# Kernel tuning notes

Hardware: AMD Instinct MI355X
Metric: run time of the kernel (lower is better)

## Reference

```python
import jax, jax.numpy as jnp
import numpy as np

D_MODEL = 4096
NUM_HEADS = 32
D_K = D_MODEL // NUM_HEADS  # 128
SEQ = D_K  # module's final `O @ scores` requires h*seq == O.shape[1] == d_model -> seq == d_k
WSCALE = 0.02


def setup_inputs() -> dict:
    key = jax.random.key(0)
    kq, kk, kv, ko, kx = jax.random.split(key, 5)
    Q = jax.random.normal(kq, (D_MODEL, D_MODEL), jnp.float32) * WSCALE
    K = jax.random.normal(kk, (D_MODEL, D_MODEL), jnp.float32) * WSCALE
    V = jax.random.normal(kv, (D_MODEL, D_MODEL), jnp.float32) * WSCALE
    O = jax.random.normal(ko, (D_MODEL, D_MODEL), jnp.float32) * WSCALE
    x = jax.random.normal(kx, (SEQ, D_MODEL), jnp.float32)
    return {"Q": Q, "K": K, "V": V, "O": O, "x": x}


def reference(Q, K, V, O, x):
    h, d = NUM_HEADS, D_K
    seq = x.shape[0]
    # stack and split weights into per-head projections: (3, h, d, d_in)
    qkv_w = jnp.stack((Q, K, V), axis=0).reshape(3, h, d, -1)
    # project: (3, h, seq, d)
    proj = jnp.einsum('phdi,si->phsd', qkv_w, x)
    q_proj, k_proj, v_proj = proj[0], proj[1], proj[2]
    # attention scores: (h, seq, seq)
    scores = jnp.einsum('hqd,hkd->hqk', q_proj, k_proj) / jnp.sqrt(jnp.asarray(d, scores_dtype := q_proj.dtype))
    # module uses triu (upper-triangular incl. diagonal) mask, multiply then fill zeros with -inf
    mask = jnp.triu(jnp.ones((seq, seq), dtype=scores.dtype))
    masked = mask * scores
    masked = jnp.where(masked == 0.0, -jnp.inf, masked)
    # stable softmax over keys (single exp, same math as subtract-max softmax)
    shifted = masked - jnp.max(masked, axis=-1, keepdims=True)
    e = jnp.exp(shifted)
    probs = e / jnp.sum(e, axis=-1, keepdims=True)
    # attention output: (h, seq, d)
    att = jnp.einsum('hqk,hkd->hqd', probs, v_proj)
    # module flattens (h, seq) together: ((h*seq), d), then left-multiplies by O
    att = att.reshape(h * seq, d)
    return O @ att  # (d_model, d_k)
```

## Files before the change

### kernel.cpp

```cpp
#include <hip/hip_runtime.h>
#include <stdint.h>

#define DM 4096

typedef __attribute__((ext_vector_type(4))) float f32x4;
typedef __attribute__((ext_vector_type(8))) short s16x8;
typedef __attribute__((ext_vector_type(8))) unsigned short u16x8;
typedef __attribute__((ext_vector_type(4))) unsigned short u16x4;

__device__ __forceinline__ unsigned short f2bf(float f) {
  union { float f; unsigned u; } c; c.f = f;
  unsigned u = c.u;
  u += 0x7FFFu + ((u >> 16) & 1u);
  return (unsigned short)(u >> 16);
}
__device__ __forceinline__ float bf2f(unsigned short h) {
  union { unsigned u; float f; } c; c.u = ((unsigned)h) << 16;
  return c.f;
}

__device__ __forceinline__ void splitbf(float v, short& hi, short& lo) {
  union { float f; unsigned u; } c; c.f = v;
  unsigned uh = c.u & 0xFFFF0000u;
  hi = (short)(uh >> 16);
  union { unsigned u; float f; } d; d.u = uh;
  lo = (short)f2bf(v - d.f);
}

__device__ __forceinline__ void wave_barrier_lgkm() {
  asm volatile("s_waitcnt lgkmcnt(0)" ::: "memory");
  __builtin_amdgcn_s_barrier();
}

__global__ __launch_bounds__(256) void k0_xsplit(const float* __restrict__ x,
                                                 unsigned short* __restrict__ xh) {
  int g = blockIdx.x * 256 + threadIdx.x;
  int kg = g & 511, s = g >> 9;
  const float* px = x + (size_t)s * DM + kg * 8;
  f32x4 v0 = *(const f32x4*)px;
  f32x4 v1 = *(const f32x4*)(px + 4);
  u16x8 hi;
#pragma unroll
  for (int j = 0; j < 8; ++j) {
    float v = (j < 4) ? v0[j] : v1[j - 4];
    hi[j] = f2bf(v);
  }
  *(u16x8*)(xh + ((size_t)kg * 128 + s) * 8) = hi;
}

__global__ __launch_bounds__(256) void k1_proj(const float* __restrict__ Q,
                                               const float* __restrict__ K,
                                               const float* __restrict__ V,
                                               const unsigned short* __restrict__ xh,
                                               float* __restrict__ pp) {
  __shared__ __align__(16) unsigned short xs[4096];
  int bid = blockIdx.x;
  int rb = bid >> 1, kc = bid & 1;
  int r0 = rb * 64;
  int w = r0 >> 12;
  int rloc = r0 & 4095;
  const float* W = (w == 0) ? Q : ((w == 1) ? K : V);
  int tid = threadIdx.x;
  int wave = tid >> 6, lane = tid & 63;
  int l15 = lane & 15, lg = lane >> 4;
  int rwb = rloc + wave * 16;
  const float* arow = W + (size_t)(rwb + l15) * DM + lg * 8;
  int kbase = kc * 2048;
  f32x4 acc[8];
#pragma unroll
  for (int i = 0; i < 8; ++i) acc[i] = (f32x4)0.f;

  u16x8 xb[4][2];
  f32x4 ab[4][2];
#pragma unroll
  for (int p = 0; p < 4; ++p) {
    int kk = kbase + p * 32;
    const u16x8* s = (const u16x8*)(xh + (size_t)kk * 128);
    xb[p][0] = s[tid];
    xb[p][1] = s[256 + tid];
    ab[p][0] = *(const f32x4*)(arow + kk);
    ab[p][1] = *(const f32x4*)(arow + kk + 4);
  }

  for (int tt = 0; tt < 16; ++tt) {
#pragma unroll
    for (int p = 0; p < 4; ++p) {
      int t = tt * 4 + p;
      wave_barrier_lgkm();
      ((u16x8*)xs)[tid] = xb[p][0];
      ((u16x8*)xs)[256 + tid] = xb[p][1];
      s16x8 Ahi, Alo;
#pragma unroll
      for (int j = 0; j < 8; ++j) {
        float v = (j < 4) ? ab[p][0][j] : ab[p][1][j - 4];
        short h, l; splitbf(v, h, l);
        Ahi[j] = h; Alo[j] = l;
      }
      int tp = t + 4;
      int kkp = kbase + ((tp < 64) ? tp : 0) * 32;
      {
        const u16x8* s = (const u16x8*)(xh + (size_t)kkp * 128);
        xb[p][0] = s[tid];
        xb[p][1] = s[256 + tid];
        ab[p][0] = *(const f32x4*)(arow + kkp);
        ab[p][1] = *(const f32x4*)(arow + kkp + 4);
      }
      wave_barrier_lgkm();
#pragma unroll
      for (int nt = 0; nt < 8; ++nt) {
        s16x8 bh = *(const s16x8*)&xs[((lg * 128) + nt * 16 + l15) * 8];
        acc[nt] = __builtin_amdgcn_mfma_f32_16x16x32_bf16(Ahi, bh, acc[nt], 0, 0, 0);
        acc[nt] = __builtin_amdgcn_mfma_f32_16x16x32_bf16(Alo, bh, acc[nt], 0, 0, 0);
      }
    }
  }

  int h = rwb >> 7;
  int dbase = (rwb & 127) + (lg << 2);
  size_t base = (size_t)(kc * 3 + w) * 524288;
  if (w < 2) {
#pragma unroll
    for (int nt = 0; nt < 8; ++nt) {
      int s = nt * 16 + l15;
      *(f32x4*)(pp + base + (size_t)(h * 128 + s) * 128 + dbase) = acc[nt];
    }
  } else {
#pragma unroll
    for (int nt = 0; nt < 8; ++nt) {
      int s = nt * 16 + l15;
#pragma unroll
      for (int r = 0; r < 4; ++r)
        pp[base + (size_t)(h * 128 + dbase + r) * 128 + s] = acc[nt][r];
    }
  }
}

__global__ __launch_bounds__(256) void k2_attn(const float* __restrict__ pp,
                                               unsigned short* __restrict__ att) {
  __shared__ __align__(16) unsigned short lds[32768];
  int h = blockIdx.x;
  int tid = threadIdx.x, wave = tid >> 6, lane = tid & 63;
  int l15 = lane & 15, lg = lane >> 4;
  const float* pk0 = pp + (size_t)1 * 524288 + (size_t)h * 16384;
  const float* pk1 = pp + (size_t)4 * 524288 + (size_t)h * 16384;
  const float* pv0 = pp + (size_t)2 * 524288 + (size_t)h * 16384;
  const float* pv1 = pp + (size_t)5 * 524288 + (size_t)h * 16384;
  for (int g = tid; g < 2048; g += 256) {
    int dg = g & 15, k = g >> 4;
    size_t so = (size_t)k * 128 + dg * 8;
    f32x4 u0 = *(const f32x4*)(pk0 + so);
    f32x4 u1 = *(const f32x4*)(pk0 + so + 4);
    f32x4 w0 = *(const f32x4*)(pk1 + so);
    f32x4 w1 = *(const f32x4*)(pk1 + so + 4);
    u16x8 kb;
#pragma unroll
    for (int j = 0; j < 4; ++j) {
      kb[j] = f2bf(u0[j] + w0[j]);
      kb[4 + j] = f2bf(u1[j] + w1[j]);
    }
    *(u16x8*)&lds[(size_t)(dg * 128 + k) * 8] = kb;
    int kg = g & 15, d = g >> 4;
    size_t vo = (size_t)d * 128 + kg * 8;
    f32x4 x0 = *(const f32x4*)(pv0 + vo);
    f32x4 x1 = *(const f32x4*)(pv0 + vo + 4);
    f32x4 y0 = *(const f32x4*)(pv1 + vo);
    f32x4 y1 = *(const f32x4*)(pv1 + vo + 4);
    u16x8 vb;
#pragma unroll
    for (int j = 0; j < 4; ++j) {
      vb[j] = f2bf(x0[j] + y0[j]);
      vb[4 + j] = f2bf(x1[j] + y1[j]);
    }
    *(u16x8*)&lds[16384 + (size_t)(kg * 128 + d) * 8] = vb;
  }
  __syncthreads();

  int qbase = wave * 32;
  const float* pq0 = pp + (size_t)h * 16384;
  const float* pq1 = pp + (size_t)3 * 524288 + (size_t)h * 16384;
  const float RS = 0.08838834764831845f;
  f32x4 sc[2][8];
#pragma unroll
  for (int a = 0; a < 2; ++a)
#pragma unroll
    for (int b = 0; b < 8; ++b) sc[a][b] = (f32x4)0.f;

  for (int ks = 0; ks < 4; ++ks) {
    s16x8 qhi[2], qlo[2];
#pragma unroll
    for (int qt = 0; qt < 2; ++qt) {
      int q = qbase + qt * 16 + l15;
      size_t qo = (size_t)q * 128 + ks * 32 + lg * 8;
      f32x4 u0 = *(const f32x4*)(pq0 + qo);
      f32x4 u1 = *(const f32x4*)(pq0 + qo + 4);
      f32x4 w0 = *(const f32x4*)(pq1 + qo);
      f32x4 w1 = *(const f32x4*)(pq1 + qo + 4);
#pragma unroll
      for (int j = 0; j < 8; ++j) {
        float v = ((j < 4) ? (u0[j] + w0[j]) : (u1[j - 4] + w1[j - 4])) * RS;
        unsigned short hh = f2bf(v);
        qhi[qt][j] = (short)hh;
        qlo[qt][j] = (short)f2bf(v - bf2f(hh));
      }
    }
#pragma unroll
    for (int nt = 0; nt < 8; ++nt) {
      s16x8 kb = *(const s16x8*)&lds[(size_t)((ks * 4 + lg) * 128 + nt * 16 + l15) * 8];
#pragma unroll
      for (int qt = 0; qt < 2; ++qt) {
        sc[qt][nt] = __builtin_amdgcn_mfma_f32_16x16x32_bf16(qhi[qt], kb, sc[qt][nt], 0, 0, 0);
        sc[qt][nt] = __builtin_amdgcn_mfma_f32_16x16x32_bf16(qlo[qt], kb, sc[qt][nt], 0, 0, 0);
      }
    }
  }
  float inv[2][4];
#pragma unroll
  for (int qt = 0; qt < 2; ++qt) {
#pragma unroll
    for (int r = 0; r < 4; ++r) {
      int q = qbase + qt * 16 + (lg << 2) + r;
      float m = -3.0e38f;
#pragma unroll
      for (int nt = 0; nt < 8; ++nt) {
        int k = nt * 16 + l15;
        float v = sc[qt][nt][r];
        if (k >= q) m = fmaxf(m, v);
      }
#pragma unroll
      for (int d = 1; d < 16; d <<= 1) m = fmaxf(m, __shfl_xor(m, d));
      float ssum = 0.f;
#pragma unroll
      for (int nt = 0; nt < 8; ++nt) {
        int k = nt * 16 + l15;
        float v = sc[qt][nt][r];
        float e = (k >= q) ? __expf(v - m) : 0.f;
        sc[qt][nt][r] = e;
        ssum += e;
      }
#pragma unroll
      for (int d = 1; d < 16; d <<= 1) ssum += __shfl_xor(ssum, d);
      inv[qt][r] = 1.f / ssum;
    }
  }
  __syncthreads();
#pragma unroll
  for (int qt = 0; qt < 2; ++qt)
#pragma unroll
    for (int nt = 0; nt < 8; ++nt) {
      int k = nt * 16 + l15;
#pragma unroll
      for (int r = 0; r < 4; ++r) {
        int q = qbase + qt * 16 + (lg << 2) + r;
        lds[(size_t)((k >> 3) * 128 + q) * 8 + (k & 7)] = f2bf(sc[qt][nt][r] * inv[qt][r]);
      }
    }
  __syncthreads();
  f32x4 o[2][8];
#pragma unroll
  for (int a = 0; a < 2; ++a)
#pragma unroll
    for (int b = 0; b < 8; ++b) o[a][b] = (f32x4)0.f;
  for (int ks = 0; ks < 4; ++ks) {
    s16x8 pa[2];
#pragma unroll
    for (int qt = 0; qt < 2; ++qt)
      pa[qt] = *(const s16x8*)&lds[(size_t)((ks * 4 + lg) * 128 + qbase + qt * 16 + l15) * 8];
#pragma unroll
    for (int nt = 0; nt < 8; ++nt) {
      s16x8 vb = *(const s16x8*)&lds[16384 + (size_t)((ks * 4 + lg) * 128 + nt * 16 + l15) * 8];
      o[0][nt] = __builtin_amdgcn_mfma_f32_16x16x32_bf16(pa[0], vb, o[0][nt], 0, 0, 0);
      o[1][nt] = __builtin_amdgcn_mfma_f32_16x16x32_bf16(pa[1], vb, o[1][nt], 0, 0, 0);
    }
  }
#pragma unroll
  for (int qt = 0; qt < 2; ++qt)
#pragma unroll
    for (int nt = 0; nt < 8; ++nt) {
      int c = nt * 16 + l15;
      int jq = h * 128 + qbase + qt * 16 + (lg << 2);
      u16x4 pk;
#pragma unroll
      for (int r = 0; r < 4; ++r) pk[r] = f2bf(o[qt][nt][r]);
      *(u16x4*)(att + (size_t)(jq >> 3) * 1024 + c * 8 + (jq & 7)) = pk;
    }
}

__global__ __launch_bounds__(256) void k3_out(const float* __restrict__ O,
                                              const unsigned short* __restrict__ att,
                                              float* __restrict__ out) {
  __shared__ __align__(16) unsigned short ats[4096];
  int bid = blockIdx.x;
  int rb = bid >> 3, kc = bid & 7;
  int r0 = rb * 64;
  int kbase = kc * 512;
  int tid = threadIdx.x, wave = tid >> 6, lane = tid & 63;
  int l15 = lane & 15, lg = lane >> 4;
  int rwb = r0 + wave * 16;
  const float* arow = O + (size_t)(rwb + l15) * DM + lg * 8;
  f32x4 acc[8];
#pragma unroll
  for (int i = 0; i < 8; ++i) acc[i] = (f32x4)0.f;

  u16x8 bb[4][2];
  f32x4 ab[4][2];
#pragma unroll
  for (int p = 0; p < 4; ++p) {
    int kk = kbase + p * 32;
    const u16x8* s = (const u16x8*)(att + (size_t)(kk >> 3) * 1024);
    bb[p][0] = s[tid];
    bb[p][1] = s[256 + tid];
    ab[p][0] = *(const f32x4*)(arow + kk);
    ab[p][1] = *(const f32x4*)(arow + kk + 4);
  }

  for (int tt = 0; tt < 4; ++tt) {
#pragma unroll
    for (int p = 0; p < 4; ++p) {
      int t = tt * 4 + p;
      wave_barrier_lgkm();
      ((u16x8*)ats)[tid] = bb[p][0];
      ((u16x8*)ats)[256 + tid] = bb[p][1];
      s16x8 Ahi, Alo;
#pragma unroll
      for (int j = 0; j < 8; ++j) {
        float v = (j < 4) ? ab[p][0][j] : ab[p][1][j - 4];
        short h, l; splitbf(v, h, l);
        Ahi[j] = h; Alo[j] = l;
      }
      int tp = t + 4;
      int kkp = kbase + ((tp < 16) ? tp : 0) * 32;
      {
        const u16x8* s = (const u16x8*)(att + (size_t)(kkp >> 3) * 1024);
        bb[p][0] = s[tid];
        bb[p][1] = s[256 + tid];
        ab[p][0] = *(const f32x4*)(arow + kkp);
        ab[p][1] = *(const f32x4*)(arow + kkp + 4);
      }
      wave_barrier_lgkm();
#pragma unroll
      for (int nt = 0; nt < 8; ++nt) {
        s16x8 bh = *(const s16x8*)&ats[((lg * 128) + nt * 16 + l15) * 8];
        acc[nt] = __builtin_amdgcn_mfma_f32_16x16x32_bf16(Ahi, bh, acc[nt], 0, 0, 0);
        acc[nt] = __builtin_amdgcn_mfma_f32_16x16x32_bf16(Alo, bh, acc[nt], 0, 0, 0);
      }
    }
  }
#pragma unroll
  for (int nt = 0; nt < 8; ++nt) {
#pragma unroll
    for (int r = 0; r < 4; ++r) {
      int row = rwb + (lg << 2) + r;
      atomicAdd(&out[(size_t)row * 128 + nt * 16 + l15], acc[nt][r]);
    }
  }
}

extern "C" void kernel_launch(void* const* d_in, const int* in_sizes, int n_in,
                              void* d_out, int out_size, void* d_ws, size_t ws_size,
                              hipStream_t stream) {
  const float* Q = (const float*)d_in[0];
  const float* K = (const float*)d_in[1];
  const float* V = (const float*)d_in[2];
  const float* O = (const float*)d_in[3];
  const float* x = (const float*)d_in[4];
  float* out = (float*)d_out;
  uint8_t* ws = (uint8_t*)d_ws;
  unsigned short* xh = (unsigned short*)ws;
  unsigned short* att = (unsigned short*)(ws + (1u << 20));
  float* pp = (float*)(ws + (2u << 20));
  hipMemsetAsync(d_out, 0, (size_t)out_size * sizeof(float), stream);
  hipLaunchKernelGGL(k0_xsplit, dim3(256), dim3(256), 0, stream, x, xh);
  hipLaunchKernelGGL(k1_proj, dim3(384), dim3(256), 0, stream, Q, K, V, xh, pp);
  hipLaunchKernelGGL(k2_attn, dim3(32), dim3(256), 0, stream, pp, att);
  hipLaunchKernelGGL(k3_out, dim3(512), dim3(256), 0, stream, O, att, out);
}
```

Before: 288.5 us.

## Drop LDS staging in GEMMs, deepen register prefetch, split attention per query block

The projection and output GEMMs stop staging the bf16 B operand through shared memory with two barriers per k-step. Each wave now loads its B fragments straight from global/L2 into double-buffered registers, and A rows are prefetched 256 columns ahead. The attention kernel is split into four query-block workgroups per head with 128 threads each, raising the grid from 32 to 128 blocks. The cost is higher register pressure (launch_bounds 256,2 may force spills), redundant global B reads per wave, and each attention block rebuilding the full K/V tile in LDS.

Result: slower. 365.1 us (+26.6%).

```diff
diff --git a/kernel.cpp b/kernel.cpp
--- a/kernel.cpp
+++ b/kernel.cpp
@@ -25,11 +25,6 @@
   hi = (short)(uh >> 16);
   union { unsigned u; float f; } d; d.u = uh;
   lo = (short)f2bf(v - d.f);
-}
-
-__device__ __forceinline__ void wave_barrier_lgkm() {
-  asm volatile("s_waitcnt lgkmcnt(0)" ::: "memory");
-  __builtin_amdgcn_s_barrier();
 }
 
 __global__ __launch_bounds__(256) void k0_xsplit(const float* __restrict__ x,
@@ -48,12 +43,11 @@
   *(u16x8*)(xh + ((size_t)kg * 128 + s) * 8) = hi;
 }
 
-__global__ __launch_bounds__(256) void k1_proj(const float* __restrict__ Q,
-                                               const float* __restrict__ K,
-                                               const float* __restrict__ V,
-                                               const unsigned short* __restrict__ xh,
-                                               float* __restrict__ pp) {
-  __shared__ __align__(16) unsigned short xs[4096];
+__global__ __launch_bounds__(256, 2) void k1_proj(const float* __restrict__ Q,
+                                                  const float* __restrict__ K,
+                                                  const float* __restrict__ V,
+                                                  const unsigned short* __restrict__ xh,
+                                                  float* __restrict__ pp) {
   int bid = blockIdx.x;
   int rb = bid >> 1, kc = bid & 1;
   int r0 = rb * 64;
@@ -65,54 +59,59 @@
   int l15 = lane & 15, lg = lane >> 4;
   int rwb = rloc + wave * 16;
   const float* arow = W + (size_t)(rwb + l15) * DM + lg * 8;
+  const s16x8* xb = (const s16x8*)xh;
   int kbase = kc * 2048;
+
   f32x4 acc[8];
 #pragma unroll
   for (int i = 0; i < 8; ++i) acc[i] = (f32x4)0.f;
-
-  u16x8 xb[4][2];
-  f32x4 ab[4][2];
-#pragma unroll
-  for (int p = 0; p < 4; ++p) {
-    int kk = kbase + p * 32;
-    const u16x8* s = (const u16x8*)(xh + (size_t)kk * 128);
-    xb[p][0] = s[tid];
-    xb[p][1] = s[256 + tid];
-    ab[p][0] = *(const f32x4*)(arow + kk);
-    ab[p][1] = *(const f32x4*)(arow + kk + 4);
-  }
-
-  for (int tt = 0; tt < 16; ++tt) {
-#pragma unroll
-    for (int p = 0; p < 4; ++p) {
-      int t = tt * 4 + p;
-      wave_barrier_lgkm();
-      ((u16x8*)xs)[tid] = xb[p][0];
-      ((u16x8*)xs)[256 + tid] = xb[p][1];
-      s16x8 Ahi, Alo;
-#pragma unroll
-      for (int j = 0; j < 8; ++j) {
-        float v = (j < 4) ? ab[p][0][j] : ab[p][1][j - 4];
-        short h, l; splitbf(v, h, l);
-        Ahi[j] = h; Alo[j] = l;
-      }
-      int tp = t + 4;
-      int kkp = kbase + ((tp < 64) ? tp : 0) * 32;
-      {
-        const u16x8* s = (const u16x8*)(xh + (size_t)kkp * 128);
-        xb[p][0] = s[tid];
-        xb[p][1] = s[256 + tid];
-        ab[p][0] = *(const f32x4*)(arow + kkp);
-        ab[p][1] = *(const f32x4*)(arow + kkp + 4);
-      }
-      wave_barrier_lgkm();
-#pragma unroll
-      for (int nt = 0; nt < 8; ++nt) {
-        s16x8 bh = *(const s16x8*)&xs[((lg * 128) + nt * 16 + l15) * 8];
-        acc[nt] = __builtin_amdgcn_mfma_f32_16x16x32_bf16(Ahi, bh, acc[nt], 0, 0, 0);
-        acc[nt] = __builtin_amdgcn_mfma_f32_16x16x32_bf16(Alo, bh, acc[nt], 0, 0, 0);
-      }
-    }
+  f32x4 aRA[16], aRB[16];
+  s16x8 bfA[8], bfB[8];
+
+  auto loadA = [&](f32x4* aR, int kss) {
+#pragma unroll
+    for (int u = 0; u < 8; ++u) {
+      aR[2 * u] = *(const f32x4*)(arow + kss + u * 32);
+      aR[2 * u + 1] = *(const f32x4*)(arow + kss + u * 32 + 4);
+    }
+  };
+  auto loadB = [&](s16x8* bf, int kk) {
+    const s16x8* bp = xb + ((size_t)(kk >> 3) + lg) * 128;
+#pragma unroll
+    for (int nt = 0; nt < 8; ++nt) bf[nt] = bp[nt * 16 + l15];
+  };
+  auto sub = [&](const f32x4& a0, const f32x4& a1, s16x8* bf) {
+    s16x8 Ahi, Alo;
+#pragma unroll
+    for (int j = 0; j < 8; ++j) {
+      float v = (j < 4) ? a0[j] : a1[j - 4];
+      short hh, ll; splitbf(v, hh, ll);
+      Ahi[j] = hh; Alo[j] = ll;
+    }
+#pragma unroll
+    for (int nt = 0; nt < 8; ++nt) {
+      acc[nt] = __builtin_amdgcn_mfma_f32_16x16x32_bf16(Ahi, bf[nt], acc[nt], 0, 0, 0);
+      acc[nt] = __builtin_amdgcn_mfma_f32_16x16x32_bf16(Alo, bf[nt], acc[nt], 0, 0, 0);
+    }
+  };
+  auto superstep = [&](f32x4* aCur, f32x4* aNxt, int kss, int kssNxt) {
+    if (kssNxt >= 0) loadA(aNxt, kssNxt);
+#pragma unroll
+    for (int u = 0; u < 8; ++u) {
+      s16x8* bc = (u & 1) ? bfB : bfA;
+      s16x8* bn = (u & 1) ? bfA : bfB;
+      int kkB = (u < 7) ? (kss + (u + 1) * 32) : (kssNxt >= 0 ? kssNxt : kss);
+      loadB(bn, kkB);
+      sub(aCur[2 * u], aCur[2 * u + 1], bc);
+    }
+  };
+
+  loadA(aRA, kbase);
+  loadB(bfA, kbase);
+  for (int sp = 0; sp < 4; ++sp) {
+    int k0s = kbase + sp * 512;
+    superstep(aRA, aRB, k0s, k0s + 256);
+    superstep(aRB, aRA, k0s + 256, (sp < 3) ? (k0s + 512) : -1);
   }
 
   int h = rwb >> 7;
@@ -135,17 +134,18 @@
   }
 }
 
-__global__ __launch_bounds__(256) void k2_attn(const float* __restrict__ pp,
+__global__ __launch_bounds__(128) void k2_attn(const float* __restrict__ pp,
                                                unsigned short* __restrict__ att) {
   __shared__ __align__(16) unsigned short lds[32768];
-  int h = blockIdx.x;
+  int bid = blockIdx.x;
+  int h = bid >> 2, qq = bid & 3;
   int tid = threadIdx.x, wave = tid >> 6, lane = tid & 63;
   int l15 = lane & 15, lg = lane >> 4;
   const float* pk0 = pp + (size_t)1 * 524288 + (size_t)h * 16384;
   const float* pk1 = pp + (size_t)4 * 524288 + (size_t)h * 16384;
   const float* pv0 = pp + (size_t)2 * 524288 + (size_t)h * 16384;
   const float* pv1 = pp + (size_t)5 * 524288 + (size_t)h * 16384;
-  for (int g = tid; g < 2048; g += 256) {
+  for (int g = tid; g < 2048; g += 128) {
     int dg = g & 15, k = g >> 4;
     size_t so = (size_t)k * 128 + dg * 8;
     f32x4 u0 = *(const f32x4*)(pk0 + so);
@@ -175,21 +175,18 @@
   }
   __syncthreads();
 
-  int qbase = wave * 32;
+  int qbase = qq * 32 + wave * 16;
   const float* pq0 = pp + (size_t)h * 16384;
   const float* pq1 = pp + (size_t)3 * 524288 + (size_t)h * 16384;
   const float RS = 0.08838834764831845f;
-  f32x4 sc[2][8];
-#pragma unroll
-  for (int a = 0; a < 2; ++a)
-#pragma unroll
-    for (int b = 0; b < 8; ++b) sc[a][b] = (f32x4)0.f;
+  f32x4 sc[8];
+#pragma unroll
+  for (int b = 0; b < 8; ++b) sc[b] = (f32x4)0.f;
 
   for (int ks = 0; ks < 4; ++ks) {
-    s16x8 qhi[2], qlo[2];
-#pragma unroll
-    for (int qt = 0; qt < 2; ++qt) {
-      int q = qbase + qt * 16 + l15;
+    s16x8 qhi, qlo;
+    {
+      int q = qbase + l15;
       size_t qo = (size_t)q * 128 + ks * 32 + lg * 8;
       f32x4 u0 = *(const f32x4*)(pq0 + qo);
       f32x4 u1 = *(const f32x4*)(pq0 + qo + 4);
@@ -199,96 +196,79 @@
       for (int j = 0; j < 8; ++j) {
         float v = ((j < 4) ? (u0[j] + w0[j]) : (u1[j - 4] + w1[j - 4])) * RS;
         unsigned short hh = f2bf(v);
-        qhi[qt][j] = (short)hh;
-        qlo[qt][j] = (short)f2bf(v - bf2f(hh));
+        qhi[j] = (short)hh;
+        qlo[j] = (short)f2bf(v - bf2f(hh));
       }
     }
 #pragma unroll
     for (int nt = 0; nt < 8; ++nt) {
       s16x8 kb = *(const s16x8*)&lds[(size_t)((ks * 4 + lg) * 128 + nt * 16 + l15) * 8];
-#pragma unroll
-      for (int qt = 0; qt < 2; ++qt) {
-        sc[qt][nt] = __builtin_amdgcn_mfma_f32_16x16x32_bf16(qhi[qt], kb, sc[qt][nt], 0, 0, 0);
-        sc[qt][nt] = __builtin_amdgcn_mfma_f32_16x16x32_bf16(qlo[qt], kb, sc[qt][nt], 0, 0, 0);
-      }
-    }
-  }
-  float inv[2][4];
-#pragma unroll
-  for (int qt = 0; qt < 2; ++qt) {
+      sc[nt] = __builtin_amdgcn_mfma_f32_16x16x32_bf16(qhi, kb, sc[nt], 0, 0, 0);
+      sc[nt] = __builtin_amdgcn_mfma_f32_16x16x32_bf16(qlo, kb, sc[nt], 0, 0, 0);
+    }
+  }
+  float inv[4];
+#pragma unroll
+  for (int r = 0; r < 4; ++r) {
+    int q = qbase + (lg << 2) + r;
+    float m = -3.0e38f;
+#pragma unroll
+    for (int nt = 0; nt < 8; ++nt) {
+      int k = nt * 16 + l15;
+      float v = sc[nt][r];
+      if (k >= q) m = fmaxf(m, v);
+    }
+#pragma unroll
+    for (int d = 1; d < 16; d <<= 1) m = fmaxf(m, __shfl_xor(m, d));
+    float ssum = 0.f;
+#pragma unroll
+    for (int nt = 0; nt < 8; ++nt) {
+      int k = nt * 16 + l15;
+      float v = sc[nt][r];
+      float e = (k >= q) ? __expf(v - m) : 0.f;
+      sc[nt][r] = e;
+      ssum += e;
+    }
+#pragma unroll
+    for (int d = 1; d < 16; d <<= 1) ssum += __shfl_xor(ssum, d);
+    inv[r] = 1.f / ssum;
+  }
+  __syncthreads();
+#pragma unroll
+  for (int nt = 0; nt < 8; ++nt) {
+    int k = nt * 16 + l15;
 #pragma unroll
     for (int r = 0; r < 4; ++r) {
-      int q = qbase + qt * 16 + (lg << 2) + r;
-      float m = -3.0e38f;
-#pragma unroll
-      for (int nt = 0; nt < 8; ++nt) {
-        int k = nt * 16 + l15;
-        float v = sc[qt][nt][r];
-        if (k >= q) m = fmaxf(m, v);
-      }
-#pragma unroll
-      for (int d = 1; d < 16; d <<= 1) m = fmaxf(m, __shfl_xor(m, d));
-      float ssum = 0.f;
-#pragma unroll
-      for (int nt = 0; nt < 8; ++nt) {
-        int k = nt * 16 + l15;
-        float v = sc[qt][nt][r];
-        float e = (k >= q) ? __expf(v - m) : 0.f;
-        sc[qt][nt][r] = e;
-        ssum += e;
-      }
-#pragma unroll
-      for (int d = 1; d < 16; d <<= 1) ssum += __shfl_xor(ssum, d);
-      inv[qt][r] = 1.f / ssum;
+      int relq = wave * 16 + (lg << 2) + r;
+      lds[(size_t)((k >> 3) * 32 + relq) * 8 + (k & 7)] = f2bf(sc[nt][r] * inv[r]);
     }
   }
   __syncthreads();
-#pragma unroll
-  for (int qt = 0; qt < 2; ++qt)
-#pragma unroll
-    for (int nt = 0; nt < 8; ++nt) {
-      int k = nt * 16 + l15;
-#pragma unroll
-      for (int r = 0; r < 4; ++r) {
-        int q = qbase + qt * 16 + (lg << 2) + r;
-        lds[(size_t)((k >> 3) * 128 + q) * 8 + (k & 7)] = f2bf(sc[qt][nt][r] * inv[qt][r]);
-      }
-    }
-  __syncthreads();
-  f32x4 o[2][8];
-#pragma unroll
-  for (int a = 0; a < 2; ++a)
-#pragma unroll
-    for (int b = 0; b < 8; ++b) o[a][b] = (f32x4)0.f;
+  f32x4 o[8];
+#pragma unroll
+  for (int b = 0; b < 8; ++b) o[b] = (f32x4)0.f;
   for (int ks = 0; ks < 4; ++ks) {
-    s16x8 pa[2];
-#pragma unroll
-    for (int qt = 0; qt < 2; ++qt)
-      pa[qt] = *(const s16x8*)&lds[(size_t)((ks * 4 + lg) * 128 + qbase + qt * 16 + l15) * 8];
+    s16x8 pa = *(const s16x8*)&lds[(size_t)((ks * 4 + lg) * 32 + wave * 16 + l15) * 8];
 #pragma unroll
     for (int nt = 0; nt < 8; ++nt) {
       s16x8 vb = *(const s16x8*)&lds[16384 + (size_t)((ks * 4 + lg) * 128 + nt * 16 + l15) * 8];
-      o[0][nt] = __builtin_amdgcn_mfma_f32_16x16x32_bf16(pa[0], vb, o[0][nt], 0, 0, 0);
-      o[1][nt] = __builtin_amdgcn_mfma_f32_16x16x32_bf16(pa[1], vb, o[1][nt], 0, 0, 0);
-    }
-  }
-#pragma unroll
-  for (int qt = 0; qt < 2; ++qt)
-#pragma unroll
-    for (int nt = 0; nt < 8; ++nt) {
-      int c = nt * 16 + l15;
-      int jq = h * 128 + qbase + qt * 16 + (lg << 2);
-      u16x4 pk;
-#pragma unroll
-      for (int r = 0; r < 4; ++r) pk[r] = f2bf(o[qt][nt][r]);
-      *(u16x4*)(att + (size_t)(jq >> 3) * 1024 + c * 8 + (jq & 7)) = pk;
-    }
-}
-
-__global__ __launch_bounds__(256) void k3_out(const float* __restrict__ O,
-                                              const unsigned short* __restrict__ att,
-                                              float* __restrict__ out) {
-  __shared__ __align__(16) unsigned short ats[4096];
+      o[nt] = __builtin_amdgcn_mfma_f32_16x16x32_bf16(pa, vb, o[nt], 0, 0, 0);
+    }
+  }
+#pragma unroll
+  for (int nt = 0; nt < 8; ++nt) {
+    int c = nt * 16 + l15;
+    int jq = h * 128 + qbase + (lg << 2);
+    u16x4 pk;
+#pragma unroll
+    for (int r = 0; r < 4; ++r) pk[r] = f2bf(o[nt][r]);
+    *(u16x4*)(att + (size_t)(jq >> 3) * 1024 + c * 8 + (jq & 7)) = pk;
+  }
+}
+
+__global__ __launch_bounds__(256, 2) void k3_out(const float* __restrict__ O,
+                                                 const unsigned short* __restrict__ att,
+                                                 float* __restrict__ out) {
   int bid = blockIdx.x;
   int rb = bid >> 3, kc = bid & 7;
   int r0 = rb * 64;
@@ -297,54 +277,57 @@
   int l15 = lane & 15, lg = lane >> 4;
   int rwb = r0 + wave * 16;
   const float* arow = O + (size_t)(rwb + l15) * DM + lg * 8;
+  const s16x8* ab = (const s16x8*)att;
+
   f32x4 acc[8];
 #pragma unroll
   for (int i = 0; i < 8; ++i) acc[i] = (f32x4)0.f;
-
-  u16x8 bb[4][2];
-  f32x4 ab[4][2];
-#pragma unroll
-  for (int p = 0; p < 4; ++p) {
-    int kk = kbase + p * 32;
-    const u16x8* s = (const u16x8*)(att + (size_t)(kk >> 3) * 1024);
-    bb[p][0] = s[tid];
-    bb[p][1] = s[256 + tid];
-    ab[p][0] = *(const f32x4*)(arow + kk);
-    ab[p][1] = *(const f32x4*)(arow + kk + 4);
-  }
-
-  for (int tt = 0; tt < 4; ++tt) {
-#pragma unroll
-    for (int p = 0; p < 4; ++p) {
-      int t = tt * 4 + p;
-      wave_barrier_lgkm();
-      ((u16x8*)ats)[tid] = bb[p][0];
-      ((u16x8*)ats)[256 + tid] = bb[p][1];
-      s16x8 Ahi, Alo;
-#pragma unroll
-      for (int j = 0; j < 8; ++j) {
-        float v = (j < 4) ? ab[p][0][j] : ab[p][1][j - 4];
-        short h, l; splitbf(v, h, l);
-        Ahi[j] = h; Alo[j] = l;
-      }
-      int tp = t + 4;
-      int kkp = kbase + ((tp < 16) ? tp : 0) * 32;
-      {
-        const u16x8* s = (const u16x8*)(att + (size_t)(kkp >> 3) * 1024);
-        bb[p][0] = s[tid];
-        bb[p][1] = s[256 + tid];
-        ab[p][0] = *(const f32x4*)(arow + kkp);
-        ab[p][1] = *(const f32x4*)(arow + kkp + 4);
-      }
-      wave_barrier_lgkm();
-#pragma unroll
-      for (int nt = 0; nt < 8; ++nt) {
-        s16x8 bh = *(const s16x8*)&ats[((lg * 128) + nt * 16 + l15) * 8];
-        acc[nt] = __builtin_amdgcn_mfma_f32_16x16x32_bf16(Ahi, bh, acc[nt], 0, 0, 0);
-        acc[nt] = __builtin_amdgcn_mfma_f32_16x16x32_bf16(Alo, bh, acc[nt], 0, 0, 0);
-      }
-    }
-  }
+  f32x4 aRA[16], aRB[16];
+  s16x8 bfA[8], bfB[8];
+
+  auto loadA = [&](f32x4* aR, int kss) {
+#pragma unroll
+    for (int u = 0; u < 8; ++u) {
+      aR[2 * u] = *(const f32x4*)(arow + kss + u * 32);
+      aR[2 * u + 1] = *(const f32x4*)(arow + kss + u * 32 + 4);
+    }
+  };
+  auto loadB = [&](s16x8* bf, int kk) {
+    const s16x8* bp = ab + ((size_t)(kk >> 3) + lg) * 128;
+#pragma unroll
+    for (int nt = 0; nt < 8; ++nt) bf[nt] = bp[nt * 16 + l15];
+  };
+  auto sub = [&](const f32x4& a0, const f32x4& a1, s16x8* bf) {
+    s16x8 Ahi, Alo;
+#pragma unroll
+    for (int j = 0; j < 8; ++j) {
+      float v = (j < 4) ? a0[j] : a1[j - 4];
+      short hh, ll; splitbf(v, hh, ll);
+      Ahi[j] = hh; Alo[j] = ll;
+    }
+#pragma unroll
+    for (int nt = 0; nt < 8; ++nt) {
+      acc[nt] = __builtin_amdgcn_mfma_f32_16x16x32_bf16(Ahi, bf[nt], acc[nt], 0, 0, 0);
+      acc[nt] = __builtin_amdgcn_mfma_f32_16x16x32_bf16(Alo, bf[nt], acc[nt], 0, 0, 0);
+    }
+  };
+  auto superstep = [&](f32x4* aCur, f32x4* aNxt, int kss, int kssNxt) {
+    if (kssNxt >= 0) loadA(aNxt, kssNxt);
+#pragma unroll
+    for (int u = 0; u < 8; ++u) {
+      s16x8* bc = (u & 1) ? bfB : bfA;
+      s16x8* bn = (u & 1) ? bfA : bfB;
+      int kkB = (u < 7) ? (kss + (u + 1) * 32) : (kssNxt >= 0 ? kssNxt : kss);
+      loadB(bn, kkB);
+      sub(aCur[2 * u], aCur[2 * u + 1], bc);
+    }
+  };
+
+  loadA(aRA, kbase);
+  loadB(bfA, kbase);
+  superstep(aRA, aRB, kbase, kbase + 256);
+  superstep(aRB, aRA, kbase + 256, -1);
+
 #pragma unroll
   for (int nt = 0; nt < 8; ++nt) {
 #pragma unroll
@@ -371,6 +354,6 @@
   hipMemsetAsync(d_out, 0, (size_t)out_size * sizeof(float), stream);
   hipLaunchKernelGGL(k0_xsplit, dim3(256), dim3(256), 0, stream, x, xh);
   hipLaunchKernelGGL(k1_proj, dim3(384), dim3(256), 0, stream, Q, K, V, xh, pp);
-  hipLaunchKernelGGL(k2_attn, dim3(32), dim3(256), 0, stream, pp, att);
+  hipLaunchKernelGGL(k2_attn, dim3(128), dim3(128), 0, stream, pp, att);
   hipLaunchKernelGGL(k3_out, dim3(512), dim3(256), 0, stream, O, att, out);
 }
```
